# Performance work log

Hardware: AMD Instinct MI355X
Metric: run time of the kernel (lower is better)

Reference implementation:

```python
import jax, jax.numpy as jnp
import numpy as np

ALPHA = 0.1        # dt / tau = 1 / 10
SIGMA_REC = 0.03
SIGMA_INP = 0.03


def setup_inputs() -> dict:
    key = jax.random.key(0)
    ks = jax.random.split(key, 7)
    n, N, num_inputs, num_outputs, T, B = 128, 1024, 6, 2, 512, 256
    u = jax.random.normal(ks[0], (num_inputs, T, B), dtype=jnp.float32)
    rec_noise = jax.random.normal(ks[1], (B, T, n), dtype=jnp.float32)
    inp_noise = jax.random.normal(ks[2], (B, T, num_inputs), dtype=jnp.float32)
    W_inp = jax.random.normal(ks[3], (n, num_inputs), dtype=jnp.float32) / np.float32(np.sqrt(num_inputs))
    # spectral-ish scaling keeps the leaky RNN stable over 512 steps
    W_rec = jax.random.normal(ks[4], (n, n), dtype=jnp.float32) * np.float32(0.9 / np.sqrt(n))
    W_out = jax.random.normal(ks[5], (num_outputs, n), dtype=jnp.float32) / np.float32(np.sqrt(n))
    # q is orthonormalized via SVD in the torch module (make_orthonormal)
    q0 = np.asarray(jax.random.uniform(ks[6], (n, N)), dtype=np.float32)
    U, _, Vh = np.linalg.svd(q0, full_matrices=False)
    q = jnp.asarray((U @ Vh).astype(np.float32))
    return dict(u=u, rec_noise=rec_noise, inp_noise=inp_noise,
                W_inp=W_inp, W_rec=W_rec, W_out=W_out, q=q)


def reference(u, rec_noise, inp_noise, W_inp, W_rec, W_out, q):
    # u: (num_inputs, T, B); noise tensors already batch-major (B, T, .)
    B = u.shape[-1]
    n = W_rec.shape[0]
    rn = jnp.sqrt(2.0 / ALPHA * SIGMA_REC ** 2) * rec_noise      # (B, T, n)
    inoise = jnp.sqrt(2.0 / ALPHA * SIGMA_INP ** 2) * inp_noise  # (B, T, num_inputs)
    ub = jnp.swapaxes(u, 0, -1)                                  # (B, T, num_inputs)
    x0 = jnp.zeros((B, n), dtype=u.dtype)                        # initial state self.x = 0

    def step(x, ins):
        u_t, in_t, rn_t = ins
        x_new = (1.0 - ALPHA) * x + ALPHA * (
            jax.nn.relu(x @ W_rec.T + (u_t + in_t) @ W_inp.T) + rn_t)
        return x_new, x_new

    # T-1 update steps using inputs at t = 0 .. T-2 (matches the torch loop)
    xs_in = (jnp.swapaxes(ub, 0, 1)[:-1],
             jnp.swapaxes(inoise, 0, 1)[:-1],
             jnp.swapaxes(rn, 0, 1)[:-1])
    _, xs = jax.lax.scan(step, x0, xs_in)                        # (T-1, B, n)
    states = jnp.concatenate([x0[:, None, :], jnp.swapaxes(xs, 0, 1)], axis=1)  # (B, T, n)

    outputs = jnp.swapaxes(states @ W_out.T, 0, -1)              # (num_outputs, T, B)
    states_embedded = jnp.swapaxes(states @ q, 0, -1)            # (N, T, B)
    return states_embedded, outputs
```

## Files before the change

### kernel.cpp

```cpp
#include <hip/hip_runtime.h>
#include <hip/hip_bf16.h>

#define T_STEPS 512
#define BATCH   256
#define NN      128
#define NEMB    1024
#define M_ROWS  (T_STEPS * BATCH)
#define NOISE_K 0.13416407864998738f

typedef short s16x8 __attribute__((ext_vector_type(8)));
typedef float f32x4 __attribute__((ext_vector_type(4)));

__device__ __forceinline__ unsigned short f2bf(float f) {
  union { float f; unsigned u; } v; v.f = f;
  unsigned r = v.u + 0x7fffu + ((v.u >> 16) & 1u);
  return (unsigned short)(r >> 16);
}
__device__ __forceinline__ float bf2f(unsigned short s) {
  union { unsigned u; float f; } v; v.u = ((unsigned)s) << 16;
  return v.f;
}

__global__ __launch_bounds__(256) void rnn_step_kernel(
    const float* __restrict__ u,
    const float* __restrict__ rec_noise,
    const float* __restrict__ inp_noise,
    const float* __restrict__ W_inp,
    const float* __restrict__ W_rec,
    unsigned short* __restrict__ states)
{
  const int b   = blockIdx.x;
  const int tid = threadIdx.x;
  const int i   = tid >> 1;
  const int h   = tid & 1;

  __shared__ float x_lds[NN];
  __shared__ float u_s[8];

  float4 w[16];
  {
    const float4* wr = (const float4*)(W_rec + i * NN + h * 64);
    #pragma unroll
    for (int c = 0; c < 16; ++c) w[c] = wr[c];
  }
  float winp[6];
  #pragma unroll
  for (int j = 0; j < 6; ++j) winp[j] = W_inp[i * 6 + j];

  if (tid < NN) x_lds[tid] = 0.f;
  if (h == 0) states[(0 * BATCH + b) * NN + i] = 0;
  __syncthreads();

  float rn_cur = rec_noise[(b * T_STEPS + 0) * NN + i];
  float uu = 0.f, in_n = 0.f;
  if (tid < 6) {
    uu   = u[tid * (T_STEPS * BATCH) + 0 * BATCH + b];
    in_n = inp_noise[(b * T_STEPS + 0) * 6 + tid];
  }

  float xr = 0.f;
  for (int t = 0; t < T_STEPS - 1; ++t) {
    if (tid < 6) u_s[tid] = uu + NOISE_K * in_n;
    float rn = rn_cur;
    if (t < T_STEPS - 2) {
      rn_cur = rec_noise[(b * T_STEPS + (t + 1)) * NN + i];
      if (tid < 6) {
        uu   = u[tid * (T_STEPS * BATCH) + (t + 1) * BATCH + b];
        in_n = inp_noise[(b * T_STEPS + (t + 1)) * 6 + tid];
      }
    }

    float acc = 0.f;
    #pragma unroll
    for (int c = 0; c < 16; ++c) {
      float4 xv = *(const float4*)&x_lds[h * 64 + c * 4];
      acc = fmaf(w[c].x, xv.x, acc);
      acc = fmaf(w[c].y, xv.y, acc);
      acc = fmaf(w[c].z, xv.z, acc);
      acc = fmaf(w[c].w, xv.w, acc);
    }
    acc += __shfl_xor(acc, 1);

    __syncthreads();

    float inp = 0.f;
    #pragma unroll
    for (int j = 0; j < 6; ++j) inp = fmaf(winp[j], u_s[j], inp);
    float pre = acc + inp;
    float r   = pre > 0.f ? pre : 0.f;
    float xn  = 0.9f * xr + 0.1f * (r + NOISE_K * rn);
    xr = xn;

    if (h == 0) {
      x_lds[i] = xn;
      states[((t + 1) * BATCH + b) * NN + i] = f2bf(xn);
    }
    __syncthreads();
  }
}

__global__ __launch_bounds__(256) void emb_kernel(
    const unsigned short* __restrict__ states,
    const float* __restrict__ q,
    float* __restrict__ out)
{
  const int jt  = blockIdx.x;
  const int mt  = blockIdx.y;
  const int tid = threadIdx.x;
  const int w   = tid >> 6;
  const int l   = tid & 63;
  const int lg  = l >> 4;
  const int lr  = l & 15;

  __shared__ unsigned short qt[64 * 128];

  {
    const int j  = tid & 63;
    const int k0 = tid >> 6;
    #pragma unroll
    for (int kk = k0; kk < 128; kk += 4) {
      float v = q[kk * NEMB + jt * 64 + j];
      int k8 = kk >> 3, e = kk & 7;
      qt[j * 128 + ((k8 ^ (j & 7)) << 3) + e] = f2bf(v);
    }
  }

  s16x8 afrag[2][4];
  #pragma unroll
  for (int mf = 0; mf < 2; ++mf) {
    const int m = mt * 128 + w * 32 + mf * 16 + lr;
    const unsigned short* arow = states + m * NN;
    #pragma unroll
    for (int kc = 0; kc < 4; ++kc)
      afrag[mf][kc] = *(const s16x8*)(arow + kc * 32 + lg * 8);
  }
  __syncthreads();

  f32x4 acc[2][4] = {};
  #pragma unroll
  for (int kc = 0; kc < 4; ++kc) {
    s16x8 bfrag[4];
    #pragma unroll
    for (int jf = 0; jf < 4; ++jf) {
      const int jl = jf * 16 + lr;
      bfrag[jf] = *(const s16x8*)(qt + jl * 128 + ((((kc << 2) + lg) ^ (jl & 7)) << 3));
    }
    #pragma unroll
    for (int mf = 0; mf < 2; ++mf)
      #pragma unroll
      for (int jf = 0; jf < 4; ++jf)
        acc[mf][jf] = __builtin_amdgcn_mfma_f32_16x16x32_bf16(
            afrag[mf][kc], bfrag[jf], acc[mf][jf], 0, 0, 0);
  }

  #pragma unroll
  for (int mf = 0; mf < 2; ++mf) {
    const int m = mt * 128 + w * 32 + mf * 16 + lg * 4;
    #pragma unroll
    for (int jf = 0; jf < 4; ++jf) {
      const long j = jt * 64 + jf * 16 + lr;
      *(f32x4*)&out[j * M_ROWS + m] = acc[mf][jf];
    }
  }
}

__global__ __launch_bounds__(256) void wout_kernel(
    const unsigned short* __restrict__ states,
    const float* __restrict__ W_out,
    float* __restrict__ out)
{
  __shared__ float wo[2 * NN];
  const int tid = threadIdx.x;
  wo[tid] = W_out[tid];
  __syncthreads();

  const int m = blockIdx.x * 256 + tid;
  const unsigned short* row = states + (size_t)m * NN;
  float a0 = 0.f, a1 = 0.f;
  #pragma unroll
  for (int c = 0; c < 16; ++c) {
    s16x8 v = *(const s16x8*)(row + c * 8);
    #pragma unroll
    for (int e = 0; e < 8; ++e) {
      float x = bf2f((unsigned short)v[e]);
      a0 = fmaf(x, wo[c * 8 + e], a0);
      a1 = fmaf(x, wo[NN + c * 8 + e], a1);
    }
  }
  out[(long)1024 * M_ROWS + m] = a0;
  out[(long)1025 * M_ROWS + m] = a1;
}

extern "C" void kernel_launch(void* const* d_in, const int* in_sizes, int n_in,
                              void* d_out, int out_size, void* d_ws, size_t ws_size,
                              hipStream_t stream) {
  const float* u         = (const float*)d_in[0];
  const float* rec_noise = (const float*)d_in[1];
  const float* inp_noise = (const float*)d_in[2];
  const float* W_inp     = (const float*)d_in[3];
  const float* W_rec     = (const float*)d_in[4];
  const float* W_out     = (const float*)d_in[5];
  const float* q         = (const float*)d_in[6];
  float* out = (float*)d_out;
  unsigned short* states = (unsigned short*)d_ws;

  rnn_step_kernel<<<dim3(BATCH), dim3(256), 0, stream>>>(
      u, rec_noise, inp_noise, W_inp, W_rec, states);

  dim3 g2(NEMB / 64, M_ROWS / 128);
  emb_kernel<<<g2, dim3(256), 0, stream>>>(states, q, out);

  wout_kernel<<<dim3(M_ROWS / 256), dim3(256), 0, stream>>>(states, W_out, out);
}
```

Before: 498.1 us.

## Double-buffer RNN state in LDS, pack two batches per block

The recurrent kernel now ping-pongs the state vector and input term between two LDS buffers, so each timestep needs only one barrier instead of two. Each 512-thread block handles two batch elements, halving the block count to 128. The dot product is split into four independent accumulators to shorten the FMA dependency chain, and the LDS layout is padded to avoid bank conflicts. In exchange, the two batches now wait on each other at every shared barrier, which could add stall time on the serial critical path.

```diff
diff --git a/kernel.cpp b/kernel.cpp
--- a/kernel.cpp
+++ b/kernel.cpp
@@ -21,7 +21,7 @@
   return v.f;
 }
 
-__global__ __launch_bounds__(256) void rnn_step_kernel(
+__global__ __launch_bounds__(512) void rnn_step_kernel(
     const float* __restrict__ u,
     const float* __restrict__ rec_noise,
     const float* __restrict__ inp_noise,
@@ -29,13 +29,15 @@
     const float* __restrict__ W_rec,
     unsigned short* __restrict__ states)
 {
-  const int b   = blockIdx.x;
   const int tid = threadIdx.x;
-  const int i   = tid >> 1;
-  const int h   = tid & 1;
-
-  __shared__ float x_lds[NN];
-  __shared__ float u_s[8];
+  const int bl  = tid >> 8;
+  const int b   = blockIdx.x * 2 + bl;
+  const int t8  = tid & 255;
+  const int i   = t8 >> 1;
+  const int h   = t8 & 1;
+
+  __shared__ float xbuf[2][2][136];
+  __shared__ float u_s[2][2][8];
 
   float4 w[16];
   {
@@ -47,54 +49,64 @@
   #pragma unroll
   for (int j = 0; j < 6; ++j) winp[j] = W_inp[i * 6 + j];
 
-  if (tid < NN) x_lds[tid] = 0.f;
+  if (t8 < 136) xbuf[bl][0][t8] = 0.f;
   if (h == 0) states[(0 * BATCH + b) * NN + i] = 0;
+
+  float rn_c = rec_noise[(b * T_STEPS + 0) * NN + i];
+  if (t8 < 6) {
+    float uu   = u[t8 * (T_STEPS * BATCH) + 0 * BATCH + b];
+    float in_n = inp_noise[(b * T_STEPS + 0) * 6 + t8];
+    u_s[bl][0][t8] = uu + NOISE_K * in_n;
+  }
   __syncthreads();
-
-  float rn_cur = rec_noise[(b * T_STEPS + 0) * NN + i];
-  float uu = 0.f, in_n = 0.f;
-  if (tid < 6) {
-    uu   = u[tid * (T_STEPS * BATCH) + 0 * BATCH + b];
-    in_n = inp_noise[(b * T_STEPS + 0) * 6 + tid];
-  }
 
   float xr = 0.f;
   for (int t = 0; t < T_STEPS - 1; ++t) {
-    if (tid < 6) u_s[tid] = uu + NOISE_K * in_n;
-    float rn = rn_cur;
-    if (t < T_STEPS - 2) {
-      rn_cur = rec_noise[(b * T_STEPS + (t + 1)) * NN + i];
-      if (tid < 6) {
-        uu   = u[tid * (T_STEPS * BATCH) + (t + 1) * BATCH + b];
-        in_n = inp_noise[(b * T_STEPS + (t + 1)) * 6 + tid];
-      }
-    }
-
-    float acc = 0.f;
-    #pragma unroll
-    for (int c = 0; c < 16; ++c) {
-      float4 xv = *(const float4*)&x_lds[h * 64 + c * 4];
-      acc = fmaf(w[c].x, xv.x, acc);
-      acc = fmaf(w[c].y, xv.y, acc);
-      acc = fmaf(w[c].z, xv.z, acc);
-      acc = fmaf(w[c].w, xv.w, acc);
-    }
+    const int cur = t & 1, nxt = cur ^ 1;
+
+    float rn_n = rec_noise[(b * T_STEPS + (t + 1)) * NN + i];
+    float uu_n = 0.f, in_nn = 0.f;
+    if (t8 < 6) {
+      uu_n  = u[t8 * (T_STEPS * BATCH) + (t + 1) * BATCH + b];
+      in_nn = inp_noise[(b * T_STEPS + (t + 1)) * 6 + t8];
+    }
+
+    const float* xb = &xbuf[bl][cur][h * 68];
+    float a0 = 0.f, a1 = 0.f, a2 = 0.f, a3 = 0.f;
+    #pragma unroll
+    for (int c = 0; c < 16; c += 4) {
+      float4 v0 = *(const float4*)&xb[(c + 0) * 4];
+      float4 v1 = *(const float4*)&xb[(c + 1) * 4];
+      float4 v2 = *(const float4*)&xb[(c + 2) * 4];
+      float4 v3 = *(const float4*)&xb[(c + 3) * 4];
+      a0 = fmaf(w[c+0].x, v0.x, a0); a0 = fmaf(w[c+0].y, v0.y, a0);
+      a0 = fmaf(w[c+0].z, v0.z, a0); a0 = fmaf(w[c+0].w, v0.w, a0);
+      a1 = fmaf(w[c+1].x, v1.x, a1); a1 = fmaf(w[c+1].y, v1.y, a1);
+      a1 = fmaf(w[c+1].z, v1.z, a1); a1 = fmaf(w[c+1].w, v1.w, a1);
+      a2 = fmaf(w[c+2].x, v2.x, a2); a2 = fmaf(w[c+2].y, v2.y, a2);
+      a2 = fmaf(w[c+2].z, v2.z, a2); a2 = fmaf(w[c+2].w, v2.w, a2);
+      a3 = fmaf(w[c+3].x, v3.x, a3); a3 = fmaf(w[c+3].y, v3.y, a3);
+      a3 = fmaf(w[c+3].z, v3.z, a3); a3 = fmaf(w[c+3].w, v3.w, a3);
+    }
+    float acc = (a0 + a1) + (a2 + a3);
     acc += __shfl_xor(acc, 1);
 
-    __syncthreads();
-
     float inp = 0.f;
     #pragma unroll
-    for (int j = 0; j < 6; ++j) inp = fmaf(winp[j], u_s[j], inp);
+    for (int j = 0; j < 6; ++j) inp = fmaf(winp[j], u_s[bl][cur][j], inp);
+
     float pre = acc + inp;
     float r   = pre > 0.f ? pre : 0.f;
-    float xn  = 0.9f * xr + 0.1f * (r + NOISE_K * rn);
+    float xn  = 0.9f * xr + 0.1f * (r + NOISE_K * rn_c);
     xr = xn;
+    rn_c = rn_n;
 
     if (h == 0) {
-      x_lds[i] = xn;
+      xbuf[bl][nxt][i + ((i >> 6) << 2)] = xn;
       states[((t + 1) * BATCH + b) * NN + i] = f2bf(xn);
     }
+    if (t8 < 6) u_s[bl][nxt][t8] = uu_n + NOISE_K * in_nn;
+
     __syncthreads();
   }
 }
@@ -204,7 +216,7 @@
   float* out = (float*)d_out;
   unsigned short* states = (unsigned short*)d_ws;
 
-  rnn_step_kernel<<<dim3(BATCH), dim3(256), 0, stream>>>(
+  rnn_step_kernel<<<dim3(BATCH / 2), dim3(512), 0, stream>>>(
       u, rec_noise, inp_noise, W_inp, W_rec, states);
 
   dim3 g2(NEMB / 64, M_ROWS / 128);
```

After: 735.3 us. +47.6%, slower.

## Chunk RNN noise/input prefetch into LDS and double-buffer state to halve barriers

Applied to the files above, without the earlier changes.

The recurrent step kernel now prefetches rec_noise and input terms for 8 timesteps at a time into double-buffered shared memory, instead of issuing per-step global loads. The state vector is ping-pong buffered with padding, so each step needs a single barrier instead of two. The dot product is split into four independent accumulators to shorten the FMA dependency chain. The cost is more LDS use and one extra barrier per chunk, and the four-accumulator split changes float summation order slightly.

```diff
diff --git a/kernel.cpp b/kernel.cpp
--- a/kernel.cpp
+++ b/kernel.cpp
@@ -7,6 +7,8 @@
 #define NEMB    1024
 #define M_ROWS  (T_STEPS * BATCH)
 #define NOISE_K 0.13416407864998738f
+#define CH      8
+#define NCHUNK  (T_STEPS / CH)
 
 typedef short s16x8 __attribute__((ext_vector_type(8)));
 typedef float f32x4 __attribute__((ext_vector_type(4)));
@@ -34,8 +36,9 @@
   const int i   = tid >> 1;
   const int h   = tid & 1;
 
-  __shared__ float x_lds[NN];
-  __shared__ float u_s[8];
+  __shared__ float xbuf[2][136];
+  __shared__ float rns[2][CH * NN];
+  __shared__ float us[2][CH][8];
 
   float4 w[16];
   {
@@ -47,55 +50,86 @@
   #pragma unroll
   for (int j = 0; j < 6; ++j) winp[j] = W_inp[i * 6 + j];
 
-  if (tid < NN) x_lds[tid] = 0.f;
-  if (h == 0) states[(0 * BATCH + b) * NN + i] = 0;
+  const int ts6 = tid / 6, j6 = tid - ts6 * 6;
+
+  if (tid < 136) xbuf[0][tid] = 0.f;
+  if (h == 0) states[b * NN + i] = 0;
+
+  {
+    const f32x4* src = (const f32x4*)(rec_noise + (size_t)b * T_STEPS * NN);
+    *(f32x4*)&rns[0][tid * 4] = src[tid];
+    if (tid < 48) {
+      float uu = u[j6 * (T_STEPS * BATCH) + ts6 * BATCH + b];
+      float in = inp_noise[((size_t)b * T_STEPS + ts6) * 6 + j6];
+      us[0][ts6][j6] = uu + NOISE_K * in;
+    }
+  }
   __syncthreads();
 
-  float rn_cur = rec_noise[(b * T_STEPS + 0) * NN + i];
-  float uu = 0.f, in_n = 0.f;
-  if (tid < 6) {
-    uu   = u[tid * (T_STEPS * BATCH) + 0 * BATCH + b];
-    in_n = inp_noise[(b * T_STEPS + 0) * 6 + tid];
-  }
-
   float xr = 0.f;
-  for (int t = 0; t < T_STEPS - 1; ++t) {
-    if (tid < 6) u_s[tid] = uu + NOISE_K * in_n;
-    float rn = rn_cur;
-    if (t < T_STEPS - 2) {
-      rn_cur = rec_noise[(b * T_STEPS + (t + 1)) * NN + i];
-      if (tid < 6) {
-        uu   = u[tid * (T_STEPS * BATCH) + (t + 1) * BATCH + b];
-        in_n = inp_noise[(b * T_STEPS + (t + 1)) * 6 + tid];
+  for (int c = 0; c < NCHUNK; ++c) {
+    const int cb = c & 1;
+
+    f32x4 rn_pf = {0.f, 0.f, 0.f, 0.f};
+    float u_pf = 0.f, in_pf = 0.f;
+    if (c < NCHUNK - 1) {
+      const f32x4* src =
+          (const f32x4*)(rec_noise + ((size_t)b * T_STEPS + (c + 1) * CH) * NN);
+      rn_pf = src[tid];
+      if (tid < 48) {
+        const int tt = (c + 1) * CH + ts6;
+        u_pf  = u[j6 * (T_STEPS * BATCH) + tt * BATCH + b];
+        in_pf = inp_noise[((size_t)b * T_STEPS + tt) * 6 + j6];
       }
     }
 
-    float acc = 0.f;
-    #pragma unroll
-    for (int c = 0; c < 16; ++c) {
-      float4 xv = *(const float4*)&x_lds[h * 64 + c * 4];
-      acc = fmaf(w[c].x, xv.x, acc);
-      acc = fmaf(w[c].y, xv.y, acc);
-      acc = fmaf(w[c].z, xv.z, acc);
-      acc = fmaf(w[c].w, xv.w, acc);
-    }
-    acc += __shfl_xor(acc, 1);
-
-    __syncthreads();
-
-    float inp = 0.f;
-    #pragma unroll
-    for (int j = 0; j < 6; ++j) inp = fmaf(winp[j], u_s[j], inp);
-    float pre = acc + inp;
-    float r   = pre > 0.f ? pre : 0.f;
-    float xn  = 0.9f * xr + 0.1f * (r + NOISE_K * rn);
-    xr = xn;
-
-    if (h == 0) {
-      x_lds[i] = xn;
-      states[((t + 1) * BATCH + b) * NN + i] = f2bf(xn);
-    }
-    __syncthreads();
+    #pragma unroll
+    for (int ts = 0; ts < CH; ++ts) {
+      const int t = c * CH + ts;
+      if (t > T_STEPS - 2) break;
+      const int cur = ts & 1, nxt = cur ^ 1;
+
+      const float* xb = &xbuf[cur][h * 68];
+      float a0 = 0.f, a1 = 0.f, a2 = 0.f, a3 = 0.f;
+      #pragma unroll
+      for (int cc = 0; cc < 16; cc += 4) {
+        float4 v0 = *(const float4*)&xb[(cc + 0) * 4];
+        float4 v1 = *(const float4*)&xb[(cc + 1) * 4];
+        float4 v2 = *(const float4*)&xb[(cc + 2) * 4];
+        float4 v3 = *(const float4*)&xb[(cc + 3) * 4];
+        a0 = fmaf(w[cc+0].x, v0.x, a0); a0 = fmaf(w[cc+0].y, v0.y, a0);
+        a0 = fmaf(w[cc+0].z, v0.z, a0); a0 = fmaf(w[cc+0].w, v0.w, a0);
+        a1 = fmaf(w[cc+1].x, v1.x, a1); a1 = fmaf(w[cc+1].y, v1.y, a1);
+        a1 = fmaf(w[cc+1].z, v1.z, a1); a1 = fmaf(w[cc+1].w, v1.w, a1);
+        a2 = fmaf(w[cc+2].x, v2.x, a2); a2 = fmaf(w[cc+2].y, v2.y, a2);
+        a2 = fmaf(w[cc+2].z, v2.z, a2); a2 = fmaf(w[cc+2].w, v2.w, a2);
+        a3 = fmaf(w[cc+3].x, v3.x, a3); a3 = fmaf(w[cc+3].y, v3.y, a3);
+        a3 = fmaf(w[cc+3].z, v3.z, a3); a3 = fmaf(w[cc+3].w, v3.w, a3);
+      }
+      float acc = (a0 + a1) + (a2 + a3);
+      acc += __shfl_xor(acc, 1);
+
+      float inp = 0.f;
+      #pragma unroll
+      for (int j = 0; j < 6; ++j) inp = fmaf(winp[j], us[cb][ts][j], inp);
+
+      const float pre = acc + inp;
+      const float r   = pre > 0.f ? pre : 0.f;
+      const float xn  = 0.9f * xr + 0.1f * (r + NOISE_K * rns[cb][ts * NN + i]);
+      xr = xn;
+
+      if (h == 0) {
+        xbuf[nxt][i + ((i >> 6) << 2)] = xn;
+        states[((t + 1) * BATCH + b) * NN + i] = f2bf(xn);
+      }
+      __syncthreads();
+    }
+
+    if (c < NCHUNK - 1) {
+      *(f32x4*)&rns[cb ^ 1][tid * 4] = rn_pf;
+      if (tid < 48) us[cb ^ 1][ts6][j6] = u_pf + NOISE_K * in_pf;
+      __syncthreads();
+    }
   }
 }
 
```

Result: faster. 470.5 us (-5.5%).
